# Optimization experiments

Hardware: AMD Instinct MI355X
Metric: run time of the kernel (lower is better)

## Reference

```python
import jax, jax.numpy as jnp
import numpy as np

N_HIDDEN = 32
RANK = 6
SV_DECAY_GAMMA = 0.3
LEAK_ALPHA = 0.1
INPUT_DIM = 64
OUTPUT_DIM = 32


def setup_inputs() -> dict:
    key = jax.random.key(0)
    ks = jax.random.split(key, 8)
    B, T = 256, 2048
    inputs = jax.random.normal(ks[0], (B, T, INPUT_DIM), dtype=jnp.float32)
    # parameters (match torch init scales)
    m = jax.random.normal(ks[1], (N_HIDDEN, 1), dtype=jnp.float32) * 0.1
    n = jax.random.normal(ks[2], (N_HIDDEN, 1), dtype=jnp.float32) * 0.1
    M = jax.random.normal(ks[3], (N_HIDDEN, RANK), dtype=jnp.float32) * 0.1
    Nmat = jax.random.normal(ks[4], (N_HIDDEN, RANK), dtype=jnp.float32) * 0.1
    # singular-value-decay scaling of M, N (as in _initialize_with_sv_decay)
    target_sv = jnp.exp(-SV_DECAY_GAMMA * jnp.arange(RANK, dtype=jnp.float32))
    target_sv = target_sv / target_sv.sum() * RANK
    sqrt_sv = jnp.sqrt(target_sv)
    M = M * sqrt_sv[None, :]
    Nmat = Nmat * sqrt_sv[None, :]
    bias = jnp.zeros((N_HIDDEN,), dtype=jnp.float32)
    # W_in: Linear(input_dim, N, bias=False) -> weight [N, input_dim]
    lim_in = 1.0 / np.sqrt(INPUT_DIM)
    W_in = jax.random.uniform(ks[5], (N_HIDDEN, INPUT_DIM), minval=-lim_in, maxval=lim_in, dtype=jnp.float32)
    lim_out = 1.0 / np.sqrt(N_HIDDEN)
    W_out = jax.random.uniform(ks[6], (OUTPUT_DIM, N_HIDDEN), minval=-lim_out, maxval=lim_out, dtype=jnp.float32)
    b_out = jax.random.uniform(ks[7], (OUTPUT_DIM,), minval=-lim_out, maxval=lim_out, dtype=jnp.float32)
    return {"inputs": inputs, "W_in": W_in, "m": m, "n": n, "M": M,
            "Nmat": Nmat, "bias": bias, "W_out": W_out, "b_out": b_out}


def reference(inputs, W_in, m, n, M, Nmat, bias, W_out, b_out):
    # h_{t+1} = (1-a) h_t + a * tanh(W_rec h_t + W_in u_t + b); y_t = W_out h_t + b_out
    B, T, _ = inputs.shape
    alpha = LEAK_ALPHA
    # W_rec = m n^T + M N^T (time-invariant; torch recomputes per step, same math)
    W_rec = m @ n.T + M @ Nmat.T                         # [N, N]
    x_proj = jnp.einsum('bti,ni->btn', inputs, W_in)     # [B, T, N]
    h0 = jnp.zeros((B, N_HIDDEN), dtype=inputs.dtype)

    def step(h, x_t):
        pre = h @ W_rec.T + x_t + bias
        h_new = (1.0 - alpha) * h + alpha * jnp.tanh(pre)
        return h_new, h_new

    h_final, hs = jax.lax.scan(step, h0, jnp.swapaxes(x_proj, 0, 1))  # hs: [T, B, N]
    outputs = jnp.einsum('tbn,on->bto', hs, W_out) + b_out            # [B, T, O]
    return outputs, h_final
```

## Files before the change

kernel.cpp:

```cpp
#include <hip/hip_runtime.h>

#define RNN_B 256
#define RNN_T 2048
#define RNN_IN 64
#define RNN_N 32
#define RNN_O 32
#define RNN_R 6
#define RNN_ALPHA 0.1f
#define KSCALE 2.8853900817779268f

__global__ __launch_bounds__(256) void k_xproj(
    const float* __restrict__ u, const float* __restrict__ W_in,
    const float* __restrict__ bias, float* __restrict__ xp)
{
    const int tid = blockIdx.x * 256 + threadIdx.x;
    const float4* __restrict__ u4 =
        reinterpret_cast<const float4*>(u) + (size_t)tid * (RNN_IN / 4);
    float acc[RNN_N];
    #pragma unroll
    for (int n = 0; n < RNN_N; ++n) acc[n] = bias[n];
    #pragma unroll
    for (int q = 0; q < RNN_IN / 4; ++q) {
        const float4 v = u4[q];
        #pragma unroll
        for (int n = 0; n < RNN_N; ++n) {
            const float* wr = W_in + n * RNN_IN + 4 * q;
            acc[n] = fmaf(wr[0], v.x, acc[n]);
            acc[n] = fmaf(wr[1], v.y, acc[n]);
            acc[n] = fmaf(wr[2], v.z, acc[n]);
            acc[n] = fmaf(wr[3], v.w, acc[n]);
        }
    }
    float4* __restrict__ o4 =
        reinterpret_cast<float4*>(xp) + (size_t)tid * (RNN_N / 4);
    #pragma unroll
    for (int q = 0; q < RNN_N / 4; ++q)
        o4[q] = make_float4(acc[4*q+0], acc[4*q+1], acc[4*q+2], acc[4*q+3]);
}

template <int CTRL>
__device__ __forceinline__ float dpp_add(float v) {
    int t = __builtin_amdgcn_update_dpp(0, __float_as_int(v), CTRL, 0xf, 0xf, true);
    return v + __int_as_float(t);
}
__device__ __forceinline__ float sum16(float v) {
    v = dpp_add<0xB1>(v);
    v = dpp_add<0x4E>(v);
    v = dpp_add<0x141>(v);
    v = dpp_add<0x140>(v);
    return v;
}

__device__ __forceinline__ float fast_exp2(float x) {
#if __has_builtin(__builtin_amdgcn_exp2f)
    return __builtin_amdgcn_exp2f(x);
#else
    return __expf(x * 0.6931471805599453f);
#endif
}
__device__ __forceinline__ float fast_rcp(float x) {
#if __has_builtin(__builtin_amdgcn_rcpf)
    return __builtin_amdgcn_rcpf(x);
#else
    return __frcp_rn(x);
#endif
}

__global__ __launch_bounds__(64, 1) void k_recur(
    const float* __restrict__ m, const float* __restrict__ nvec,
    const float* __restrict__ Mmat, const float* __restrict__ Nmat,
    float* __restrict__ dout, float* __restrict__ hfin)
{
    const int b    = blockIdx.x;
    const int lane = threadIdx.x;
    const int k    = lane & 15;
    const int kB   = k + 16;

    float cNA[RNN_R + 1], cNB[RNN_R + 1];
    cNA[0] = nvec[k];  cNB[0] = nvec[kB];
    #pragma unroll
    for (int r = 0; r < RNN_R; ++r) { cNA[r+1] = Mmat ? Nmat[k*RNN_R + r] : 0.f; cNB[r+1] = Nmat[kB*RNN_R + r]; }
    float cMA[RNN_R + 1], cMB[RNN_R + 1];
    cMA[0] = KSCALE * m[k];  cMB[0] = KSCALE * m[kB];
    #pragma unroll
    for (int r = 0; r < RNN_R; ++r) { cMA[r+1] = KSCALE * Mmat[k*RNN_R + r]; cMB[r+1] = KSCALE * Mmat[kB*RNN_R + r]; }

    float* __restrict__ base = dout + (size_t)b * (RNN_T * RNN_N);
    float hA = 0.0f, hB = 0.0f;

    const int PF = 4;
    float xrA[PF], xrB[PF];
    #pragma unroll
    for (int i = 0; i < PF; ++i) {
        xrA[i] = base[i * RNN_N + k];
        xrB[i] = base[i * RNN_N + kB];
    }

    #pragma unroll 4
    for (int t = 0; t < RNN_T; ++t) {
        const float xA = xrA[0], xB = xrB[0];
        xrA[0] = xrA[1]; xrA[1] = xrA[2]; xrA[2] = xrA[3];
        xrB[0] = xrB[1]; xrB[1] = xrB[2]; xrB[2] = xrB[3];
        xrA[PF - 1] = base[(t + PF) * RNN_N + k];
        xrB[PF - 1] = base[(t + PF) * RNN_N + kB];

        float s[RNN_R + 1];
        #pragma unroll
        for (int r = 0; r < RNN_R + 1; ++r)
            s[r] = sum16(fmaf(hB, cNB[r], hA * cNA[r]));

        float zA0 = fmaf(cMA[0], s[0], KSCALE * xA);
        float zB0 = fmaf(cMB[0], s[0], KSCALE * xB);
        float zA1 = cMA[1] * s[1];
        float zB1 = cMB[1] * s[1];
        zA0 = fmaf(cMA[2], s[2], zA0);  zB0 = fmaf(cMB[2], s[2], zB0);
        zA1 = fmaf(cMA[3], s[3], zA1);  zB1 = fmaf(cMB[3], s[3], zB1);
        zA0 = fmaf(cMA[4], s[4], zA0);  zB0 = fmaf(cMB[4], s[4], zB0);
        zA1 = fmaf(cMA[5], s[5], zA1);  zB1 = fmaf(cMB[5], s[5], zB1);
        zA0 = fmaf(cMA[6], s[6], zA0);  zB0 = fmaf(cMB[6], s[6], zB0);
        const float zA = zA0 + zA1, zB = zB0 + zB1;

        const float eA = fast_exp2(zA), eB = fast_exp2(zB);
        const float gA = fmaf(1.0f - RNN_ALPHA, hA, RNN_ALPHA);
        const float gB = fmaf(1.0f - RNN_ALPHA, hB, RNN_ALPHA);
        hA = fmaf(-2.0f * RNN_ALPHA, fast_rcp(eA + 1.0f), gA);
        hB = fmaf(-2.0f * RNN_ALPHA, fast_rcp(eB + 1.0f), gB);

        const float hs = (lane < 16) ? hA : hB;
        if (lane < RNN_N) base[t * RNN_N + lane] = hs;
    }
    const float hs = (lane < 16) ? hA : hB;
    if (lane < RNN_N) hfin[b * RNN_N + lane] = hs;
}

__global__ __launch_bounds__(256) void k_out(
    const float* __restrict__ W_out, const float* __restrict__ b_out,
    float* __restrict__ dout)
{
    const int tid = blockIdx.x * 256 + threadIdx.x;
    float4* __restrict__ p4 =
        reinterpret_cast<float4*>(dout) + (size_t)tid * (RNN_N / 4);
    float y[RNN_O];
    #pragma unroll
    for (int o = 0; o < RNN_O; ++o) y[o] = b_out[o];
    #pragma unroll
    for (int q = 0; q < RNN_N / 4; ++q) {
        const float4 v = p4[q];
        #pragma unroll
        for (int o = 0; o < RNN_O; ++o) {
            const float* wr = W_out + o * RNN_N + 4 * q;
            y[o] = fmaf(wr[0], v.x, y[o]);
            y[o] = fmaf(wr[1], v.y, y[o]);
            y[o] = fmaf(wr[2], v.z, y[o]);
            y[o] = fmaf(wr[3], v.w, y[o]);
        }
    }
    #pragma unroll
    for (int q = 0; q < RNN_N / 4; ++q)
        p4[q] = make_float4(y[4*q+0], y[4*q+1], y[4*q+2], y[4*q+3]);
}

extern "C" void kernel_launch(void* const* d_in, const int* in_sizes, int n_in,
                              void* d_out, int out_size, void* d_ws, size_t ws_size,
                              hipStream_t stream)
{
    const float* u     = (const float*)d_in[0];
    const float* W_in  = (const float*)d_in[1];
    const float* m     = (const float*)d_in[2];
    const float* nvec  = (const float*)d_in[3];
    const float* Mmat  = (const float*)d_in[4];
    const float* Nmat  = (const float*)d_in[5];
    const float* bias  = (const float*)d_in[6];
    const float* W_out = (const float*)d_in[7];
    const float* b_out = (const float*)d_in[8];
    float* out = (float*)d_out;

    float* hfin = out + (size_t)RNN_B * RNN_T * RNN_N;

    k_xproj<<<(RNN_B * RNN_T) / 256, 256, 0, stream>>>(u, W_in, bias, out);
    k_recur<<<RNN_B, 64, 0, stream>>>(m, nvec, Mmat, Nmat, out, hfin);
    k_out  <<<(RNN_B * RNN_T) / 256, 256, 0, stream>>>(W_out, b_out, out);
}
```

Before: 739.1 us.

## Interleave hidden units per lane, vectorize recurrence I/O, separate hidden buffer

Each lane now handles hidden units 2k and 2k+1 instead of k and k+16, so x-projection reads and hidden-state writes become single float2 accesses by 16 lanes. The prefetch depth rises from 4 to 8 steps to hide global-load latency on the serial recurrence. The KSCALE multiply moves into the projection kernel, taking one multiply off the per-step chain. Hidden states go to a workspace buffer when one is available, so the output kernel no longer reads and writes the same array in place. Costs: more registers for the deeper prefetch and a dependence on workspace size.

```diff
diff --git a/kernel.cpp b/kernel.cpp
--- a/kernel.cpp
+++ b/kernel.cpp
@@ -35,7 +35,8 @@
         reinterpret_cast<float4*>(xp) + (size_t)tid * (RNN_N / 4);
     #pragma unroll
     for (int q = 0; q < RNN_N / 4; ++q)
-        o4[q] = make_float4(acc[4*q+0], acc[4*q+1], acc[4*q+2], acc[4*q+3]);
+        o4[q] = make_float4(KSCALE * acc[4*q+0], KSCALE * acc[4*q+1],
+                            KSCALE * acc[4*q+2], KSCALE * acc[4*q+3]);
 }
 
 template <int CTRL>
@@ -69,48 +70,57 @@
 __global__ __launch_bounds__(64, 1) void k_recur(
     const float* __restrict__ m, const float* __restrict__ nvec,
     const float* __restrict__ Mmat, const float* __restrict__ Nmat,
-    float* __restrict__ dout, float* __restrict__ hfin)
+    const float* __restrict__ xp,
+    float* __restrict__ hout,
+    float* __restrict__ hfin)
 {
     const int b    = blockIdx.x;
     const int lane = threadIdx.x;
     const int k    = lane & 15;
-    const int kB   = k + 16;
+    const int iA   = 2 * k;
+    const int iB   = 2 * k + 1;
 
     float cNA[RNN_R + 1], cNB[RNN_R + 1];
-    cNA[0] = nvec[k];  cNB[0] = nvec[kB];
+    cNA[0] = nvec[iA];  cNB[0] = nvec[iB];
     #pragma unroll
-    for (int r = 0; r < RNN_R; ++r) { cNA[r+1] = Mmat ? Nmat[k*RNN_R + r] : 0.f; cNB[r+1] = Nmat[kB*RNN_R + r]; }
+    for (int r = 0; r < RNN_R; ++r) {
+        cNA[r+1] = Nmat[iA*RNN_R + r];
+        cNB[r+1] = Nmat[iB*RNN_R + r];
+    }
     float cMA[RNN_R + 1], cMB[RNN_R + 1];
-    cMA[0] = KSCALE * m[k];  cMB[0] = KSCALE * m[kB];
+    cMA[0] = KSCALE * m[iA];  cMB[0] = KSCALE * m[iB];
     #pragma unroll
-    for (int r = 0; r < RNN_R; ++r) { cMA[r+1] = KSCALE * Mmat[k*RNN_R + r]; cMB[r+1] = KSCALE * Mmat[kB*RNN_R + r]; }
+    for (int r = 0; r < RNN_R; ++r) {
+        cMA[r+1] = KSCALE * Mmat[iA*RNN_R + r];
+        cMB[r+1] = KSCALE * Mmat[iB*RNN_R + r];
+    }
 
-    float* __restrict__ base = dout + (size_t)b * (RNN_T * RNN_N);
+    const float2* __restrict__ x2 =
+        reinterpret_cast<const float2*>(xp + (size_t)b * (RNN_T * RNN_N)) + k;
+    float2* __restrict__ h2 =
+        reinterpret_cast<float2*>(hout + (size_t)b * (RNN_T * RNN_N));
+
     float hA = 0.0f, hB = 0.0f;
 
-    const int PF = 4;
-    float xrA[PF], xrB[PF];
+    const int PF = 8;
+    float2 xr[PF];
     #pragma unroll
-    for (int i = 0; i < PF; ++i) {
-        xrA[i] = base[i * RNN_N + k];
-        xrB[i] = base[i * RNN_N + kB];
-    }
+    for (int i = 0; i < PF; ++i) xr[i] = x2[i * (RNN_N / 2)];
 
-    #pragma unroll 4
+    #pragma unroll 8
     for (int t = 0; t < RNN_T; ++t) {
-        const float xA = xrA[0], xB = xrB[0];
-        xrA[0] = xrA[1]; xrA[1] = xrA[2]; xrA[2] = xrA[3];
-        xrB[0] = xrB[1]; xrB[1] = xrB[2]; xrB[2] = xrB[3];
-        xrA[PF - 1] = base[(t + PF) * RNN_N + k];
-        xrB[PF - 1] = base[(t + PF) * RNN_N + kB];
+        const float xA = xr[0].x, xB = xr[0].y;
+        #pragma unroll
+        for (int i = 0; i < PF - 1; ++i) xr[i] = xr[i + 1];
+        xr[PF - 1] = x2[(t + PF) * (RNN_N / 2)];
 
         float s[RNN_R + 1];
         #pragma unroll
         for (int r = 0; r < RNN_R + 1; ++r)
             s[r] = sum16(fmaf(hB, cNB[r], hA * cNA[r]));
 
-        float zA0 = fmaf(cMA[0], s[0], KSCALE * xA);
-        float zB0 = fmaf(cMB[0], s[0], KSCALE * xB);
+        float zA0 = fmaf(cMA[0], s[0], xA);
+        float zB0 = fmaf(cMB[0], s[0], xB);
         float zA1 = cMA[1] * s[1];
         float zB1 = cMB[1] * s[1];
         zA0 = fmaf(cMA[2], s[2], zA0);  zB0 = fmaf(cMB[2], s[2], zB0);
@@ -126,20 +136,22 @@
         hA = fmaf(-2.0f * RNN_ALPHA, fast_rcp(eA + 1.0f), gA);
         hB = fmaf(-2.0f * RNN_ALPHA, fast_rcp(eB + 1.0f), gB);
 
-        const float hs = (lane < 16) ? hA : hB;
-        if (lane < RNN_N) base[t * RNN_N + lane] = hs;
+        if (lane < 16) h2[t * (RNN_N / 2) + lane] = make_float2(hA, hB);
     }
-    const float hs = (lane < 16) ? hA : hB;
-    if (lane < RNN_N) hfin[b * RNN_N + lane] = hs;
+    if (lane < 16)
+        reinterpret_cast<float2*>(hfin + (size_t)b * RNN_N)[lane] =
+            make_float2(hA, hB);
 }
 
 __global__ __launch_bounds__(256) void k_out(
     const float* __restrict__ W_out, const float* __restrict__ b_out,
-    float* __restrict__ dout)
+    const float* __restrict__ hsrc, float* __restrict__ ydst)
 {
     const int tid = blockIdx.x * 256 + threadIdx.x;
-    float4* __restrict__ p4 =
-        reinterpret_cast<float4*>(dout) + (size_t)tid * (RNN_N / 4);
+    const float4* __restrict__ p4 =
+        reinterpret_cast<const float4*>(hsrc) + (size_t)tid * (RNN_N / 4);
+    float4* __restrict__ q4 =
+        reinterpret_cast<float4*>(ydst) + (size_t)tid * (RNN_N / 4);
     float y[RNN_O];
     #pragma unroll
     for (int o = 0; o < RNN_O; ++o) y[o] = b_out[o];
@@ -157,7 +169,7 @@
     }
     #pragma unroll
     for (int q = 0; q < RNN_N / 4; ++q)
-        p4[q] = make_float4(y[4*q+0], y[4*q+1], y[4*q+2], y[4*q+3]);
+        q4[q] = make_float4(y[4*q+0], y[4*q+1], y[4*q+2], y[4*q+3]);
 }
 
 extern "C" void kernel_launch(void* const* d_in, const int* in_sizes, int n_in,
@@ -177,7 +189,10 @@
 
     float* hfin = out + (size_t)RNN_B * RNN_T * RNN_N;
 
+    const size_t hbytes = (size_t)RNN_B * RNN_T * RNN_N * sizeof(float);
+    float* hbuf = (ws_size >= hbytes) ? (float*)d_ws : out;
+
     k_xproj<<<(RNN_B * RNN_T) / 256, 256, 0, stream>>>(u, W_in, bias, out);
-    k_recur<<<RNN_B, 64, 0, stream>>>(m, nvec, Mmat, Nmat, out, hfin);
-    k_out  <<<(RNN_B * RNN_T) / 256, 256, 0, stream>>>(W_out, b_out, out);
+    k_recur<<<RNN_B, 64, 0, stream>>>(m, nvec, Mmat, Nmat, out, hbuf, hfin);
+    k_out  <<<(RNN_B * RNN_T) / 256, 256, 0, stream>>>(W_out, b_out, hbuf, out);
 }
```

Result: faster. 713.4 us (-3.5%).
